# Kernel tuning notes

Hardware: AMD Instinct MI355X
Metric: run time of the kernel (lower is better)

The kernel has to match this reference:

```python
import jax, jax.numpy as jnp
import numpy as np

D_MODEL, D_K, D_V, H = 1024, 64, 64, 16
B, NQ, NK = 8, 1024, 1024


def setup_inputs() -> dict:
    key = jax.random.key(0)
    ks = jax.random.split(key, 12)
    s = 0.02
    queries = jax.random.normal(ks[0], (B, NQ, D_MODEL), jnp.float32)
    keys_ = jax.random.normal(ks[1], (B, NK, D_MODEL), jnp.float32)
    values = jax.random.normal(ks[2], (B, NK, D_MODEL), jnp.float32)
    attention_weights = jax.random.uniform(ks[3], (B, H, NQ, NK), jnp.float32)
    # causal mask: True = masked; strict upper triangle so no row is fully masked
    attention_mask = ~jnp.tril(jnp.ones((NQ, NK), dtype=bool))[None, None]
    Wq = jax.random.normal(ks[4], (H * D_K, D_MODEL), jnp.float32) * s
    Wk = jax.random.normal(ks[5], (H * D_K, D_MODEL), jnp.float32) * s
    Wv = jax.random.normal(ks[6], (H * D_V, D_MODEL), jnp.float32) * s
    Wo = jax.random.normal(ks[7], (D_MODEL, H * D_V), jnp.float32) * s
    bq = jnp.zeros((H * D_K,), jnp.float32)
    bk = jnp.zeros((H * D_K,), jnp.float32)
    bv = jnp.zeros((H * D_V,), jnp.float32)
    bo = jnp.zeros((D_MODEL,), jnp.float32)
    return dict(queries=queries, keys=keys_, values=values,
                attention_weights=attention_weights, attention_mask=attention_mask,
                Wq=Wq, bq=bq, Wk=Wk, bk=bk, Wv=Wv, bv=bv, Wo=Wo, bo=bo)


def reference(queries, keys, values, attention_weights, attention_mask,
              Wq, bq, Wk, bk, Wv, bv, Wo, bo):
    b_s, nq, _ = queries.shape
    nk = keys.shape[1]
    # torch Linear: y = x @ W.T + b
    q = (queries @ Wq.T + bq).reshape(b_s, nq, H, D_K).transpose(0, 2, 1, 3)  # b h q d
    k = (keys @ Wk.T + bk).reshape(b_s, nk, H, D_K).transpose(0, 2, 1, 3)     # b h k d
    v = (values @ Wv.T + bv).reshape(b_s, nk, H, D_V).transpose(0, 2, 1, 3)   # b h k d
    att = jnp.einsum('bhqd,bhkd->bhqk', q, k) / np.sqrt(D_K).astype(np.float32)
    att = att * attention_weights
    att = jnp.where(attention_mask, -jnp.inf, att)
    att = jax.nn.softmax(att, axis=-1)
    out = jnp.einsum('bhqk,bhkd->bqhd', att, v).reshape(b_s, nq, H * D_V)
    return out @ Wo.T + bo
```

## Files before the change

kernel.cpp:

```cpp
#include <hip/hip_runtime.h>


typedef unsigned short u16;
typedef __attribute__((ext_vector_type(8))) short short8;
typedef __attribute__((ext_vector_type(4))) float float4v;

__device__ __forceinline__ u16 f2bf(float f) {
    unsigned int u = __float_as_uint(f);
    u = (u + 0x7fffu + ((u >> 16) & 1u)) >> 16;
    return (u16)u;
}

__device__ __forceinline__ void glds16(const void* g, void* l) {
    __builtin_amdgcn_global_load_lds(
        (const __attribute__((address_space(1))) unsigned int*)g,
        (__attribute__((address_space(3))) unsigned int*)l, 16, 0, 0);
}

__global__ __launch_bounds__(256) void convert_bf16(const float* s0, const float* s1,
                                                    const float* s2, const float* s3,
                                                    const float* s4, const float* s5,
                                                    const float* s6, u16* base) {
    const size_t offs[7] = {0, 8388608, 16777216, 25165824, 26214400, 27262976, 28311552};
    const int    ns[7]   = {8388608, 8388608, 8388608, 1048576, 1048576, 1048576, 1048576};
    const float* srcs[7] = {s0, s1, s2, s3, s4, s5, s6};
    const int t = blockIdx.y;
    const float* src = srcs[t];
    u16* dst = base + offs[t];
    const int n8 = ns[t] >> 3;
    const int stride = gridDim.x * 256;
    for (int i = blockIdx.x * 256 + threadIdx.x; i < n8; i += stride) {
        float4 a = ((const float4*)src)[i * 2];
        float4 b = ((const float4*)src)[i * 2 + 1];
        uint4 o;
        o.x = (unsigned)f2bf(a.x) | ((unsigned)f2bf(a.y) << 16);
        o.y = (unsigned)f2bf(a.z) | ((unsigned)f2bf(a.w) << 16);
        o.z = (unsigned)f2bf(b.x) | ((unsigned)f2bf(b.y) << 16);
        o.w = (unsigned)f2bf(b.z) | ((unsigned)f2bf(b.w) << 16);
        ((uint4*)dst)[i] = o;
    }
}

template <bool OUT_BF16>
__global__ __launch_bounds__(256) void gemm_bt(const u16* __restrict__ Ab,
                                               const u16* __restrict__ Wb,
                                               const float* b0, const float* b1,
                                               const float* b2, void* Cb,
                                               size_t Astride, size_t Wstride,
                                               size_t Cstride) {
    __shared__ __align__(16) u16 As[8192];
    __shared__ __align__(16) u16 Bs[8192];

    const int z = blockIdx.z;
    const u16* A = Ab + (size_t)z * Astride;
    const u16* W = Wb + (size_t)z * Wstride;
    const float* bias = (z == 0) ? b0 : (z == 1) ? b1 : b2;

    const int m0 = blockIdx.x * 128, n0 = blockIdx.y * 128;
    const int tid = threadIdx.x, lane = tid & 63, w = tid >> 6;
    const int wm = (w & 1) * 64, wn = (w >> 1) * 64;
    const int c = lane & 15, quad = lane >> 4;
    const int srow = tid >> 3;
    const int scol = (tid & 7) * 8;

    float4v acc[4][4] = {};

    for (int kb = 0; kb < 1024; kb += 64) {
#pragma unroll
        for (int i = 0; i < 4; ++i) {
            glds16(&A[(size_t)(m0 + i * 32 + srow) * 1024 + kb + scol], &As[i * 2048 + w * 512]);
            glds16(&W[(size_t)(n0 + i * 32 + srow) * 1024 + kb + scol], &Bs[i * 2048 + w * 512]);
        }
        __syncthreads();
#pragma unroll
        for (int ks = 0; ks < 2; ++ks) {
            short8 a[4], b[4];
#pragma unroll
            for (int i = 0; i < 4; ++i)
                a[i] = *(const short8*)&As[(wm + i * 16 + c) * 64 + ks * 32 + quad * 8];
#pragma unroll
            for (int j = 0; j < 4; ++j)
                b[j] = *(const short8*)&Bs[(wn + j * 16 + c) * 64 + ks * 32 + quad * 8];
#pragma unroll
            for (int i = 0; i < 4; ++i)
#pragma unroll
                for (int j = 0; j < 4; ++j)
                    acc[i][j] = __builtin_amdgcn_mfma_f32_16x16x32_bf16(a[i], b[j], acc[i][j], 0, 0, 0);
        }
        __syncthreads();
    }

#pragma unroll
    for (int j = 0; j < 4; ++j) {
        int n = n0 + wn + j * 16 + c;
        float bv = bias[n];
#pragma unroll
        for (int i = 0; i < 4; ++i) {
            int mb = m0 + wm + i * 16 + quad * 4;
#pragma unroll
            for (int r = 0; r < 4; ++r) {
                float v = acc[i][j][r] + bv;
                size_t off = (size_t)(mb + r) * 1024 + n;
                if (OUT_BF16) ((u16*)Cb + (size_t)z * Cstride)[off] = f2bf(v);
                else          ((float*)Cb)[off] = v;
            }
        }
    }
}

__global__ __launch_bounds__(256) void transpose_v(const u16* __restrict__ Vb,
                                                   u16* __restrict__ Vt) {
    __shared__ __align__(16) u16 t[64][72];
    const int bh = blockIdx.y, b = bh >> 4, h = bh & 15;
    const int k0 = blockIdx.x * 64;
    const int tid = threadIdx.x;
    {
        int key = tid >> 2, d0 = (tid & 3) << 4;
        const uint4* src = (const uint4*)&Vb[(size_t)(b * 1024 + k0 + key) * 1024 + h * 64 + d0];
        *(uint4*)&t[key][d0]     = src[0];
        *(uint4*)&t[key][d0 + 8] = src[1];
    }
    __syncthreads();
    {
        int d = tid & 63, kg = (tid >> 6) << 4;
        uint4 o[2];
        u16* op = (u16*)o;
#pragma unroll
        for (int i = 0; i < 16; ++i) op[i] = t[kg + i][d];
        uint4* dst = (uint4*)&Vt[((size_t)bh * 64 + d) * 1024 + k0 + kg];
        dst[0] = o[0];
        dst[1] = o[1];
    }
}

__global__ __launch_bounds__(256) void attn_kernel(const u16* __restrict__ Qb,
                                                   const u16* __restrict__ Kb,
                                                   const u16* __restrict__ Vt,
                                                   const float* __restrict__ Wts,
                                                   u16* __restrict__ AO) {
    __shared__ __align__(16) u16 Ks[4096];
    __shared__ __align__(16) u16 Vs[4096];
    __shared__ __align__(16) u16 Pl[4][1024];

    const int qt = blockIdx.x;
    const int bh = blockIdx.y;
    const int b = bh >> 4, h = bh & 15;
    const int q0 = qt * 64;
    const int tid = threadIdx.x, lane = tid & 63, w = tid >> 6;
    const int c = lane & 15, quad = lane >> 4;
    const int qrow = q0 + w * 16;
    const int srow = tid >> 3, scol = (tid & 7) * 8;

    short8 qf[2];
#pragma unroll
    for (int ks = 0; ks < 2; ++ks)
        qf[ks] = *(const short8*)&Qb[(size_t)(b * 1024 + qrow + c) * 1024 + h * 64 + ks * 32 + quad * 8];

    float m_run[4], l_run[4];
    float4v o[4] = {};
#pragma unroll
    for (int r = 0; r < 4; ++r) { m_run[r] = -1e30f; l_run[r] = 0.f; }

    for (int kt = 0; kt <= qt; ++kt) {
        const int k0 = kt * 64;
#pragma unroll
        for (int i = 0; i < 2; ++i) {
            glds16(&Kb[(size_t)(b * 1024 + k0 + i * 32 + srow) * 1024 + h * 64 + scol],
                   &Ks[i * 2048 + w * 512]);
            glds16(&Vt[((size_t)bh * 64 + i * 32 + srow) * 1024 + k0 + scol],
                   &Vs[i * 2048 + w * 512]);
        }
        float wv[4][4];
        const float* wp = &Wts[((size_t)bh * 1024 + (qrow + quad * 4)) * 1024 + k0 + c];
#pragma unroll
        for (int t = 0; t < 4; ++t)
#pragma unroll
            for (int r = 0; r < 4; ++r) wv[t][r] = wp[(size_t)r * 1024 + t * 16];
        __syncthreads();
        float4v s[4] = {};
#pragma unroll
        for (int ks = 0; ks < 2; ++ks)
#pragma unroll
            for (int t = 0; t < 4; ++t) {
                short8 kf = *(const short8*)&Ks[(t * 16 + c) * 64 + ks * 32 + quad * 8];
                s[t] = __builtin_amdgcn_mfma_f32_16x16x32_bf16(qf[ks], kf, s[t], 0, 0, 0);
            }
        const bool diag = (kt == qt);
#pragma unroll
        for (int t = 0; t < 4; ++t)
#pragma unroll
            for (int r = 0; r < 4; ++r) {
                float v = s[t][r] * 0.125f * wv[t][r];
                if (diag && (k0 + t * 16 + c) > (qrow + quad * 4 + r)) v = -1e30f;
                s[t][r] = v;
            }
        float alpha[4];
#pragma unroll
        for (int r = 0; r < 4; ++r) {
            float v = fmaxf(fmaxf(s[0][r], s[1][r]), fmaxf(s[2][r], s[3][r]));
#pragma unroll
            for (int off = 1; off < 16; off <<= 1) v = fmaxf(v, __shfl_xor(v, off, 64));
            float mn = fmaxf(m_run[r], v);
            alpha[r] = __expf(m_run[r] - mn);
            m_run[r] = mn;
        }
#pragma unroll
        for (int r = 0; r < 4; ++r) {
            float sum = 0.f;
#pragma unroll
            for (int t = 0; t < 4; ++t) {
                float p = __expf(s[t][r] - m_run[r]);
                s[t][r] = p;
                sum += p;
            }
#pragma unroll
            for (int off = 1; off < 16; off <<= 1) sum += __shfl_xor(sum, off, 64);
            l_run[r] = l_run[r] * alpha[r] + sum;
        }
#pragma unroll
        for (int t = 0; t < 4; ++t)
#pragma unroll
            for (int r = 0; r < 4; ++r)
                Pl[w][(quad * 4 + r) * 64 + t * 16 + c] = f2bf(s[t][r]);
#pragma unroll
        for (int dt = 0; dt < 4; ++dt)
#pragma unroll
            for (int r = 0; r < 4; ++r) o[dt][r] *= alpha[r];
#pragma unroll
        for (int ks = 0; ks < 2; ++ks) {
            short8 pf = *(const short8*)&Pl[w][c * 64 + ks * 32 + quad * 8];
#pragma unroll
            for (int dt = 0; dt < 4; ++dt) {
                short8 vf = *(const short8*)&Vs[(dt * 16 + c) * 64 + ks * 32 + quad * 8];
                o[dt] = __builtin_amdgcn_mfma_f32_16x16x32_bf16(pf, vf, o[dt], 0, 0, 0);
            }
        }
        __syncthreads();
    }
#pragma unroll
    for (int dt = 0; dt < 4; ++dt)
#pragma unroll
        for (int r = 0; r < 4; ++r)
            AO[(size_t)(b * 1024 + qrow + quad * 4 + r) * 1024 + h * 64 + dt * 16 + c] =
                f2bf(o[dt][r] / l_run[r]);
}

extern "C" void kernel_launch(void* const* d_in, const int* in_sizes, int n_in,
                              void* d_out, int out_size, void* d_ws, size_t ws_size,
                              hipStream_t stream) {
    const float* q  = (const float*)d_in[0];
    const float* k  = (const float*)d_in[1];
    const float* v  = (const float*)d_in[2];
    const float* aw = (const float*)d_in[3];
    const float* bq = (const float*)d_in[6];
    const float* bk = (const float*)d_in[8];
    const float* bv = (const float*)d_in[10];
    const float* Wo = (const float*)d_in[11];
    const float* bo = (const float*)d_in[12];
    const float* Wq = (const float*)d_in[5];
    const float* Wk = (const float*)d_in[7];
    const float* Wv = (const float*)d_in[9];

    u16* ws16 = (u16*)d_ws;
    u16* qkvbf = ws16;
    u16* Wbf   = ws16 + 25165824;
    u16* Wob   = ws16 + 28311552;
    u16* Qb    = ws16 + 29360128;
    u16* Kb    = Qb + 8388608;
    u16* Vb    = Kb + 8388608;
    u16* Vt    = Vb + 8388608;
    u16* AObf  = Vt + 8388608;

    dim3 blk(256);
    convert_bf16<<<dim3(512, 7), blk, 0, stream>>>(q, k, v, Wq, Wk, Wv, Wo, ws16);
    gemm_bt<true><<<dim3(64, 8, 3), blk, 0, stream>>>(qkvbf, Wbf, bq, bk, bv, Qb,
                                                      8388608, 1048576, 8388608);
    transpose_v<<<dim3(16, 128), blk, 0, stream>>>(Vb, Vt);
    attn_kernel<<<dim3(16, 128), blk, 0, stream>>>(Qb, Kb, Vt, aw, AObf);
    gemm_bt<false><<<dim3(64, 8, 1), blk, 0, stream>>>(AObf, Wob, bo, bo, bo, d_out,
                                                       0, 0, 0);
}
```

Before: 957.0 us.

## Replace GEMM with 256x256 double-buffered, swizzled 8-wave pipelined kernel

Swaps the 128x128 single-buffered projection GEMM for a 256x256-tile, 512-thread kernel. It double-buffers LDS tiles, prefetching the next K-tile via global_load_lds interleaved with MFMA phases, and XOR-swizzles LDS columns to reduce bank conflicts. s_setprio raises wave priority during MFMA bursts. Larger tiles raise data reuse but shrink the grid (384 and 128 blocks) and use 128KB LDS per block, which may limit occupancy and tail balance.

Measured after the change: 949.2 us. No clear change (-0.8%).

```diff
diff --git a/kernel.cpp b/kernel.cpp
--- a/kernel.cpp
+++ b/kernel.cpp
@@ -15,6 +15,12 @@
     __builtin_amdgcn_global_load_lds(
         (const __attribute__((address_space(1))) unsigned int*)g,
         (__attribute__((address_space(3))) unsigned int*)l, 16, 0, 0);
+}
+
+__device__ __forceinline__ void bar() {
+    asm volatile("" ::: "memory");
+    __builtin_amdgcn_s_barrier();
+    asm volatile("" ::: "memory");
 }
 
 __global__ __launch_bounds__(256) void convert_bf16(const float* s0, const float* s1,
@@ -42,64 +48,146 @@
 }
 
 template <bool OUT_BF16>
-__global__ __launch_bounds__(256) void gemm_bt(const u16* __restrict__ Ab,
-                                               const u16* __restrict__ Wb,
-                                               const float* b0, const float* b1,
-                                               const float* b2, void* Cb,
-                                               size_t Astride, size_t Wstride,
-                                               size_t Cstride) {
-    __shared__ __align__(16) u16 As[8192];
-    __shared__ __align__(16) u16 Bs[8192];
+__global__ __launch_bounds__(512, 2) void gemm_bt8(const u16* __restrict__ Ab,
+                                                   const u16* __restrict__ Wb,
+                                                   const float* b0, const float* b1,
+                                                   const float* b2, void* Cb,
+                                                   size_t Astride, size_t Wstride,
+                                                   size_t Cstride) {
+    __shared__ __align__(16) u16 As[32768];
+    __shared__ __align__(16) u16 Bs[32768];
 
     const int z = blockIdx.z;
     const u16* A = Ab + (size_t)z * Astride;
     const u16* W = Wb + (size_t)z * Wstride;
     const float* bias = (z == 0) ? b0 : (z == 1) ? b1 : b2;
 
-    const int m0 = blockIdx.x * 128, n0 = blockIdx.y * 128;
-    const int tid = threadIdx.x, lane = tid & 63, w = tid >> 6;
-    const int wm = (w & 1) * 64, wn = (w >> 1) * 64;
-    const int c = lane & 15, quad = lane >> 4;
+    const int m0 = blockIdx.x * 256, n0 = blockIdx.y * 256;
+    const int tid = threadIdx.x, lane = tid & 63, ww = tid >> 6;
+    const int wm = ww & 1, wn = ww >> 1;
+    const int c = lane & 15, quad = (lane >> 4) & 3;
+
     const int srow = tid >> 3;
-    const int scol = (tid & 7) * 8;
-
-    float4v acc[4][4] = {};
-
-    for (int kb = 0; kb < 1024; kb += 64) {
-#pragma unroll
-        for (int i = 0; i < 4; ++i) {
-            glds16(&A[(size_t)(m0 + i * 32 + srow) * 1024 + kb + scol], &As[i * 2048 + w * 512]);
-            glds16(&W[(size_t)(n0 + i * 32 + srow) * 1024 + kb + scol], &Bs[i * 2048 + w * 512]);
-        }
-        __syncthreads();
-#pragma unroll
-        for (int ks = 0; ks < 2; ++ks) {
-            short8 a[4], b[4];
-#pragma unroll
-            for (int i = 0; i < 4; ++i)
-                a[i] = *(const short8*)&As[(wm + i * 16 + c) * 64 + ks * 32 + quad * 8];
-#pragma unroll
-            for (int j = 0; j < 4; ++j)
-                b[j] = *(const short8*)&Bs[(wn + j * 16 + c) * 64 + ks * 32 + quad * 8];
-#pragma unroll
-            for (int i = 0; i < 4; ++i)
-#pragma unroll
-                for (int j = 0; j < 4; ++j)
-                    acc[i][j] = __builtin_amdgcn_mfma_f32_16x16x32_bf16(a[i], b[j], acc[i][j], 0, 0, 0);
-        }
-        __syncthreads();
-    }
-
-#pragma unroll
-    for (int j = 0; j < 4; ++j) {
-        int n = n0 + wn + j * 16 + c;
+    const int scol = ((tid & 7) ^ (srow & 7)) << 3;
+    const int wbase = ww << 9;
+
+    auto stA = [&](int slot, int cc, int kt) {
+        glds16(&A[(size_t)(m0 + cc * 64 + srow) * 1024 + kt * 64 + scol],
+               &As[slot * 16384 + cc * 4096 + wbase]);
+    };
+    auto stB = [&](int slot, int cc, int kt) {
+        glds16(&W[(size_t)(n0 + cc * 64 + srow) * 1024 + kt * 64 + scol],
+               &Bs[slot * 16384 + cc * 4096 + wbase]);
+    };
+    auto ldA = [&](int slot, int mh, int mi, int ks) -> short8 {
+        int row = wm * 128 + mh * 64 + mi * 16 + c;
+        int ch = ((ks << 2) + quad) ^ (c & 7);
+        return *(const short8*)&As[slot * 16384 + row * 64 + ch * 8];
+    };
+    auto ldB = [&](int slot, int nh, int ni, int ks) -> short8 {
+        int row = wn * 64 + nh * 32 + ni * 16 + c;
+        int ch = ((ks << 2) + quad) ^ (c & 7);
+        return *(const short8*)&Bs[slot * 16384 + row * 64 + ch * 8];
+    };
+
+    float4v acc[8][4] = {};
+
+    stB(0, 0, 0); stB(0, 1, 0); stB(0, 2, 0); stB(0, 3, 0);
+    stA(0, 0, 0); stA(0, 2, 0); stA(0, 1, 0); stA(0, 3, 0);
+    asm volatile("s_waitcnt vmcnt(2)" ::: "memory");
+    bar();
+
+    auto step = [&](int t, int slot, bool pre) {
+        const int nxt = slot ^ 1;
+        short8 af0[4][2], af1[4][2], bf[2][2][2];
+#pragma unroll
+        for (int mi = 0; mi < 4; ++mi)
+#pragma unroll
+            for (int ks = 0; ks < 2; ++ks) af0[mi][ks] = ldA(slot, 0, mi, ks);
+#pragma unroll
+        for (int ni = 0; ni < 2; ++ni)
+#pragma unroll
+            for (int ks = 0; ks < 2; ++ks) bf[0][ni][ks] = ldB(slot, 0, ni, ks);
+        if (pre) { stB(nxt, 0, t + 1); stB(nxt, 1, t + 1); }
+        bar();
+        __builtin_amdgcn_s_setprio(1);
+#pragma unroll
+        for (int mi = 0; mi < 4; ++mi)
+#pragma unroll
+            for (int ni = 0; ni < 2; ++ni)
+#pragma unroll
+                for (int ks = 0; ks < 2; ++ks)
+                    acc[mi][ni] = __builtin_amdgcn_mfma_f32_16x16x32_bf16(
+                        af0[mi][ks], bf[0][ni][ks], acc[mi][ni], 0, 0, 0);
+        __builtin_amdgcn_s_setprio(0);
+        bar();
+#pragma unroll
+        for (int ni = 0; ni < 2; ++ni)
+#pragma unroll
+            for (int ks = 0; ks < 2; ++ks) bf[1][ni][ks] = ldB(slot, 1, ni, ks);
+        if (pre) { stB(nxt, 2, t + 1); stB(nxt, 3, t + 1); }
+        bar();
+        __builtin_amdgcn_s_setprio(1);
+#pragma unroll
+        for (int mi = 0; mi < 4; ++mi)
+#pragma unroll
+            for (int ni = 0; ni < 2; ++ni)
+#pragma unroll
+                for (int ks = 0; ks < 2; ++ks)
+                    acc[mi][2 + ni] = __builtin_amdgcn_mfma_f32_16x16x32_bf16(
+                        af0[mi][ks], bf[1][ni][ks], acc[mi][2 + ni], 0, 0, 0);
+        __builtin_amdgcn_s_setprio(0);
+        if (pre) { asm volatile("s_waitcnt vmcnt(4)" ::: "memory"); }
+        else     { asm volatile("s_waitcnt vmcnt(0)" ::: "memory"); }
+        bar();
+#pragma unroll
+        for (int mi = 0; mi < 4; ++mi)
+#pragma unroll
+            for (int ks = 0; ks < 2; ++ks) af1[mi][ks] = ldA(slot, 1, mi, ks);
+        if (pre) { stA(nxt, 0, t + 1); stA(nxt, 2, t + 1); }
+        bar();
+        __builtin_amdgcn_s_setprio(1);
+#pragma unroll
+        for (int mi = 0; mi < 4; ++mi)
+#pragma unroll
+            for (int ni = 0; ni < 2; ++ni)
+#pragma unroll
+                for (int ks = 0; ks < 2; ++ks)
+                    acc[4 + mi][ni] = __builtin_amdgcn_mfma_f32_16x16x32_bf16(
+                        af1[mi][ks], bf[0][ni][ks], acc[4 + mi][ni], 0, 0, 0);
+        __builtin_amdgcn_s_setprio(0);
+        bar();
+        if (pre) { stA(nxt, 1, t + 1); stA(nxt, 3, t + 1); }
+        bar();
+        __builtin_amdgcn_s_setprio(1);
+#pragma unroll
+        for (int mi = 0; mi < 4; ++mi)
+#pragma unroll
+            for (int ni = 0; ni < 2; ++ni)
+#pragma unroll
+                for (int ks = 0; ks < 2; ++ks)
+                    acc[4 + mi][2 + ni] = __builtin_amdgcn_mfma_f32_16x16x32_bf16(
+                        af1[mi][ks], bf[1][ni][ks], acc[4 + mi][2 + ni], 0, 0, 0);
+        __builtin_amdgcn_s_setprio(0);
+        asm volatile("s_waitcnt vmcnt(2)" ::: "memory");
+        bar();
+    };
+
+    for (int th = 0; th < 8; ++th) {
+        step(2 * th, 0, true);
+        step(2 * th + 1, 1, th < 7);
+    }
+
+#pragma unroll
+    for (int bj = 0; bj < 4; ++bj) {
+        int n = n0 + wn * 64 + (bj >> 1) * 32 + (bj & 1) * 16 + c;
         float bv = bias[n];
 #pragma unroll
-        for (int i = 0; i < 4; ++i) {
-            int mb = m0 + wm + i * 16 + quad * 4;
+        for (int ai = 0; ai < 8; ++ai) {
+            int mb = m0 + wm * 128 + (ai >> 2) * 64 + (ai & 3) * 16 + quad * 4;
 #pragma unroll
             for (int r = 0; r < 4; ++r) {
-                float v = acc[i][j][r] + bv;
+                float v = acc[ai][bj][r] + bv;
                 size_t off = (size_t)(mb + r) * 1024 + n;
                 if (OUT_BF16) ((u16*)Cb + (size_t)z * Cstride)[off] = f2bf(v);
                 else          ((float*)Cb)[off] = v;
@@ -273,10 +361,10 @@
 
     dim3 blk(256);
     convert_bf16<<<dim3(512, 7), blk, 0, stream>>>(q, k, v, Wq, Wk, Wv, Wo, ws16);
-    gemm_bt<true><<<dim3(64, 8, 3), blk, 0, stream>>>(qkvbf, Wbf, bq, bk, bv, Qb,
-                                                      8388608, 1048576, 8388608);
+    gemm_bt8<true><<<dim3(32, 4, 3), dim3(512), 0, stream>>>(qkvbf, Wbf, bq, bk, bv, Qb,
+                                                             8388608, 1048576, 8388608);
     transpose_v<<<dim3(16, 128), blk, 0, stream>>>(Vb, Vt);
     attn_kernel<<<dim3(16, 128), blk, 0, stream>>>(Qb, Kb, Vt, aw, AObf);
-    gemm_bt<false><<<dim3(64, 8, 1), blk, 0, stream>>>(AObf, Wob, bo, bo, bo, d_out,
-                                                       0, 0, 0);
-}
+    gemm_bt8<false><<<dim3(32, 4, 1), dim3(512), 0, stream>>>(AObf, Wob, bo, bo, bo, d_out,
+                                                              0, 0, 0);
+}
```
